# Kernel optimization log

Measured on AMD Instinct MI355X. Metric: run time of the kernel, lower is better.

## Reference

```python
import jax, jax.numpy as jnp
import numpy as np

DIM = 4096
N_EXPERTS = 256
TOPK = 8
N_GROUPS = 8
TOPK_GROUPS = 4
ROUTE_SCALE = 2.5
N_TOKENS = 16384


def setup_inputs() -> dict:
    key = jax.random.key(0)
    k1, k2 = jax.random.split(key)
    x = jax.random.normal(k1, (N_TOKENS, DIM), dtype=jnp.float32)
    weight = jax.random.normal(k2, (N_EXPERTS, DIM), dtype=jnp.float32) * 0.01
    e_score_correction_bias = jnp.zeros((N_EXPERTS,), dtype=jnp.float32)
    return {"x": x, "weight": weight, "e_score_correction_bias": e_score_correction_bias}


def reference(x, weight, e_score_correction_bias):
    n = x.shape[0]
    # [n, E] expert scores
    scores = jax.nn.sigmoid(jnp.dot(x, weight.T))
    original_scores = scores
    scores = scores + e_score_correction_bias
    # group selection: top-2 sum per group -> top-k groups
    scores_g = scores.reshape(n, N_GROUPS, -1)  # [n, G, E/G]
    group_score = jnp.sort(scores_g, axis=-1)[..., -2:].sum(axis=-1)  # [n, G]
    group_idx = jnp.argsort(group_score, axis=-1)[..., -TOPK_GROUPS:]  # [n, kg]
    mask = jnp.ones((n, N_GROUPS), dtype=bool)
    mask = mask.at[jnp.arange(n)[:, None], group_idx].set(False)
    scores_masked = jnp.where(mask[..., None], -jnp.inf, scores_g).reshape(n, -1)
    # final top-k experts
    indices = jnp.argsort(scores_masked, axis=-1)[..., -TOPK:]  # [n, k]
    weights = original_scores[jnp.arange(n)[:, None], indices]  # [n, k]
    weights = weights / (weights.sum(axis=-1, keepdims=True) + 1e-20)
    weights = weights * ROUTE_SCALE
    return (weights, indices)
```

## Files before the change

### kernel.cpp

```cpp
#include <hip/hip_runtime.h>
#include <math.h>

#define DIMK 4096
#define NEXP 256
#define BM   64
#define BK32 32
#define NT   (DIMK / BK32)
#define NGRP 8
#define GSZ  32
#define TOPKG 4
#define TOPKE 8
#define BTILE 49152
#define WS_NEED ((size_t)NT * BTILE)

#define XTILE   12288
#define SMEM_SZ 131584

typedef __bf16 bf16x8 __attribute__((ext_vector_type(8)));
typedef float f32x4 __attribute__((ext_vector_type(4)));

__device__ __forceinline__ void decomp8(const float v[8], uint4& H, uint4& M, uint4& L) {
  union U { __bf16 b[8]; uint4 u; } h, m, l;
#pragma unroll
  for (int i = 0; i < 8; ++i) {
    float xv = v[i];
    __bf16 hb = (__bf16)xv;
    float r1 = xv - (float)hb;
    __bf16 mb = (__bf16)r1;
    float r2 = r1 - (float)mb;
    h.b[i] = hb; m.b[i] = mb; l.b[i] = (__bf16)r2;
  }
  H = h.u; M = m.u; L = l.u;
}

__device__ __forceinline__ void decomp4(float4 v, uint2& H, uint2& M, uint2& L) {
  union U { __bf16 b[4]; uint2 u; } h, m, l;
  float vv[4] = {v.x, v.y, v.z, v.w};
#pragma unroll
  for (int i = 0; i < 4; ++i) {
    float xv = vv[i];
    __bf16 hb = (__bf16)xv;
    float r1 = xv - (float)hb;
    __bf16 mb = (__bf16)r1;
    float r2 = r1 - (float)mb;
    h.b[i] = hb; m.b[i] = mb; l.b[i] = (__bf16)r2;
  }
  H = h.u; M = m.u; L = l.u;
}

__global__ __launch_bounds__(256) void w_split_kernel(const float* __restrict__ wgt,
                                                      unsigned char* __restrict__ ws) {
  const int g = blockIdx.x * 256 + threadIdx.x;
  const int e = g >> 9;
  const int k0 = (g & 511) << 3;
  const int kt = k0 >> 5;
  const int chunk = (k0 & 31) >> 3;
  const int lane = chunk * 16 + (e & 15);
  const int eb = e >> 4;
  float v[8];
  float4 a = *(const float4*)(wgt + (long)e * DIMK + k0);
  float4 b = *(const float4*)(wgt + (long)e * DIMK + k0 + 4);
  v[0]=a.x; v[1]=a.y; v[2]=a.z; v[3]=a.w; v[4]=b.x; v[5]=b.y; v[6]=b.z; v[7]=b.w;
  uint4 H, M, L;
  decomp8(v, H, M, L);
  const long base = ((long)(kt * 3) * 16 + eb) * 1024 + lane * 16;
  *(uint4*)(ws + base)             = H;
  *(uint4*)(ws + base + 16 * 1024) = M;
  *(uint4*)(ws + base + 32 * 1024) = L;
}

__global__ __launch_bounds__(512) void moe_gate_mfma(
    const float* __restrict__ x, const unsigned char* __restrict__ ws,
    const float* __restrict__ bias, float* __restrict__ outw, float* __restrict__ outi) {
  __shared__ __align__(16) unsigned char smem[SMEM_SZ];
  double* sc = (double*)smem;

  const int tid = threadIdx.x;
  const int lane = tid & 63;
  const int l15 = lane & 15;
  const int wid = tid >> 6;
  const int wr = wid >> 2;
  const int wc = wid & 3;
  const long bm0 = (long)blockIdx.x * BM;

  const int xtok = tid >> 3;
  const int xq = tid & 7;
  const float* xptr = x + (bm0 + xtok) * (long)DIMK + xq * 4;
  const int xwoff = (xq >> 1) * 1024 + xtok * 16 + (xq & 1) * 8;

  const unsigned char* wsb = ws + (wc * 4) * 1024 + lane * 16;

  f32x4 D[2][4];
  double acc[2][4][4];
#pragma unroll
  for (int rt = 0; rt < 2; ++rt)
#pragma unroll
    for (int ct = 0; ct < 4; ++ct) {
      D[rt][ct] = (f32x4){0.f, 0.f, 0.f, 0.f};
#pragma unroll
      for (int r = 0; r < 4; ++r) acc[rt][ct][r] = 0.0;
    }

  float4 xv;
  bf16x8 bh0, bh1, bh2, bh3, bm0r, bm1r, bm2r, bm3r, bl0, bl1, bl2, bl3;

  bh0 = *(const bf16x8*)(wsb + 0 * 16384 + 0 * 1024);
  bh1 = *(const bf16x8*)(wsb + 0 * 16384 + 1 * 1024);
  bh2 = *(const bf16x8*)(wsb + 0 * 16384 + 2 * 1024);
  bh3 = *(const bf16x8*)(wsb + 0 * 16384 + 3 * 1024);
  bm0r = *(const bf16x8*)(wsb + 1 * 16384 + 0 * 1024);
  bm1r = *(const bf16x8*)(wsb + 1 * 16384 + 1 * 1024);
  bm2r = *(const bf16x8*)(wsb + 1 * 16384 + 2 * 1024);
  bm3r = *(const bf16x8*)(wsb + 1 * 16384 + 3 * 1024);
  bl0 = *(const bf16x8*)(wsb + 2 * 16384 + 0 * 1024);
  bl1 = *(const bf16x8*)(wsb + 2 * 16384 + 1 * 1024);
  bl2 = *(const bf16x8*)(wsb + 2 * 16384 + 2 * 1024);
  bl3 = *(const bf16x8*)(wsb + 2 * 16384 + 3 * 1024);
  xv = *(const float4*)(xptr);
  {
    uint2 H, M, L;
    decomp4(xv, H, M, L);
    *(uint2*)(smem + xwoff + 0 * 4096) = H;
    *(uint2*)(smem + xwoff + 1 * 4096) = M;
    *(uint2*)(smem + xwoff + 2 * 4096) = L;
  }
  __syncthreads();

#define MM(A, B, RT, CT) \
  D[RT][CT] = __builtin_amdgcn_mfma_f32_16x16x32_bf16(A, B, D[RT][CT], 0, 0, 0)
#define P8(A0, A1, B0, B1, B2, B3) \
  MM(A0, B0, 0, 0); MM(A0, B1, 0, 1); MM(A0, B2, 0, 2); MM(A0, B3, 0, 3); \
  MM(A1, B0, 1, 0); MM(A1, B1, 1, 1); MM(A1, B2, 1, 2); MM(A1, B3, 1, 3)

  long bo_n = BTILE;

#pragma unroll 1
  for (int t = 0; t < NT; ++t) {
    const int buf = t & 1, nbuf = buf ^ 1;
    const bool more = (t + 1 < NT);
    if (more) xv = *(const float4*)(xptr + (t + 1) * BK32);
    const unsigned char* xb = smem + buf * XTILE;
    const int ao0 = (lane >> 4) * 1024 + (wr * 32 + l15) * 16;
    const int ao1 = ao0 + 256;
    bf16x8 ah0 = *(const bf16x8*)(xb + 0 * 4096 + ao0);
    bf16x8 ah1 = *(const bf16x8*)(xb + 0 * 4096 + ao1);
    bf16x8 am0 = *(const bf16x8*)(xb + 1 * 4096 + ao0);
    bf16x8 am1 = *(const bf16x8*)(xb + 1 * 4096 + ao1);
    bf16x8 al0 = *(const bf16x8*)(xb + 2 * 4096 + ao0);
    bf16x8 al1 = *(const bf16x8*)(xb + 2 * 4096 + ao1);
    __builtin_amdgcn_s_setprio(1);
    P8(ah0, ah1, bh0, bh1, bh2, bh3);
    P8(am0, am1, bh0, bh1, bh2, bh3);
    P8(al0, al1, bh0, bh1, bh2, bh3);
    bh0 = *(const bf16x8*)(wsb + bo_n + 0 * 16384 + 0 * 1024);
    bh1 = *(const bf16x8*)(wsb + bo_n + 0 * 16384 + 1 * 1024);
    bh2 = *(const bf16x8*)(wsb + bo_n + 0 * 16384 + 2 * 1024);
    bh3 = *(const bf16x8*)(wsb + bo_n + 0 * 16384 + 3 * 1024);
    P8(ah0, ah1, bm0r, bm1r, bm2r, bm3r);
    P8(am0, am1, bm0r, bm1r, bm2r, bm3r);
    bm0r = *(const bf16x8*)(wsb + bo_n + 1 * 16384 + 0 * 1024);
    bm1r = *(const bf16x8*)(wsb + bo_n + 1 * 16384 + 1 * 1024);
    bm2r = *(const bf16x8*)(wsb + bo_n + 1 * 16384 + 2 * 1024);
    bm3r = *(const bf16x8*)(wsb + bo_n + 1 * 16384 + 3 * 1024);
    P8(ah0, ah1, bl0, bl1, bl2, bl3);
    bl0 = *(const bf16x8*)(wsb + bo_n + 2 * 16384 + 0 * 1024);
    bl1 = *(const bf16x8*)(wsb + bo_n + 2 * 16384 + 1 * 1024);
    bl2 = *(const bf16x8*)(wsb + bo_n + 2 * 16384 + 2 * 1024);
    bl3 = *(const bf16x8*)(wsb + bo_n + 2 * 16384 + 3 * 1024);
    __builtin_amdgcn_s_setprio(0);
    if (more) {
      uint2 H, M, L;
      decomp4(xv, H, M, L);
      unsigned char* xw = smem + nbuf * XTILE + xwoff;
      *(uint2*)(xw + 0 * 4096) = H;
      *(uint2*)(xw + 1 * 4096) = M;
      *(uint2*)(xw + 2 * 4096) = L;
    }
    if (t & 1) {
#pragma unroll
      for (int rt = 0; rt < 2; ++rt)
#pragma unroll
        for (int ct = 0; ct < 4; ++ct) {
#pragma unroll
          for (int r = 0; r < 4; ++r) acc[rt][ct][r] += (double)D[rt][ct][r];
          D[rt][ct] = (f32x4){0.f, 0.f, 0.f, 0.f};
        }
    }
    __syncthreads();
    if (t + 2 < NT) bo_n += BTILE;
  }
#undef P8
#undef MM

#pragma unroll
  for (int rt = 0; rt < 2; ++rt)
#pragma unroll
    for (int ct = 0; ct < 4; ++ct) {
      const int col = wc * 64 + ct * 16 + l15;
      const double bd = (double)bias[col];
#pragma unroll
      for (int r = 0; r < 4; ++r) {
        const int row = wr * 32 + rt * 16 + (lane >> 4) * 4 + r;
        const double s = 1.0 / (1.0 + exp(-acc[rt][ct][r]));
        sc[row * 257 + col] = s + bd;
      }
    }
  __syncthreads();

  if (tid < BM) {
    double* row = sc + tid * 257;
    double gs[NGRP];
#pragma unroll
    for (int g = 0; g < NGRP; ++g) {
      double m1 = -1e300, m2 = -1e300;
      for (int e = 0; e < GSZ; ++e) {
        double v = row[g * GSZ + e];
        if (v > m1) { m2 = m1; m1 = v; }
        else if (v > m2) { m2 = v; }
      }
      gs[g] = m1 + m2;
    }
    unsigned msk = 0;
#pragma unroll
    for (int g = 0; g < NGRP; ++g) {
      int cnt = 0;
#pragma unroll
      for (int h = 0; h < NGRP; ++h)
        cnt += ((gs[h] > gs[g]) || (gs[h] == gs[g] && h > g)) ? 1 : 0;
      if (cnt < TOPKG) msk |= (1u << g);
    }
    int g0 = __ffs(msk) - 1; msk &= msk - 1;
    int g1 = __ffs(msk) - 1; msk &= msk - 1;
    int g2 = __ffs(msk) - 1; msk &= msk - 1;
    int g3 = __ffs(msk) - 1;

    double wv[TOPKE];
    float iv[TOPKE];
#pragma unroll
    for (int r8 = 0; r8 < TOPKE; ++r8) {
      double best = -1e300;
      int bi = 0;
      {
        int gg = g0;
        for (int e = 0; e < GSZ; ++e) { double v = row[gg * GSZ + e]; if (v >= best) { best = v; bi = gg * GSZ + e; } }
        gg = g1;
        for (int e = 0; e < GSZ; ++e) { double v = row[gg * GSZ + e]; if (v >= best) { best = v; bi = gg * GSZ + e; } }
        gg = g2;
        for (int e = 0; e < GSZ; ++e) { double v = row[gg * GSZ + e]; if (v >= best) { best = v; bi = gg * GSZ + e; } }
        gg = g3;
        for (int e = 0; e < GSZ; ++e) { double v = row[gg * GSZ + e]; if (v >= best) { best = v; bi = gg * GSZ + e; } }
      }
      row[bi] = -1e300;
      wv[7 - r8] = best - (double)bias[bi];
      iv[7 - r8] = (float)bi;
    }
    double sum = 0.0;
#pragma unroll
    for (int p = 0; p < TOPKE; ++p) sum += wv[p];
    const double den = sum + 1e-20;
    const long trow = bm0 + tid;
#pragma unroll
    for (int p = 0; p < TOPKE; ++p) {
      outw[trow * 8 + p] = (float)(wv[p] / den * 2.5);
      outi[trow * 8 + p] = iv[p];
    }
  }
}

#define BMF  64
#define BKF 16
#define LXSF 68
__global__ __launch_bounds__(256, 1) void moe_gate_f64(
    const float* __restrict__ x, const float* __restrict__ wgt,
    const float* __restrict__ bias, float* __restrict__ outw,
    float* __restrict__ outi) {
  __shared__ __align__(16) unsigned char smem[64 * 257 * 8];
  float* lw = (float*)smem;
  float* lx = (float*)(smem + 32768);
  double* sc = (double*)smem;
  const int tid = threadIdx.x;
  const long bm0 = (long)blockIdx.x * BMF;
  const int rg = tid >> 5;
  const int cg = tid & 31;
  const int sxr = tid >> 2;
  const int sxj = (tid & 3) << 2;
  const float* xrow = x + (bm0 + sxr) * (long)DIMK + sxj;
  const float* wrow = wgt + (long)tid * DIMK;
  double acc[8][8];
#pragma unroll
  for (int i = 0; i < 8; ++i)
#pragma unroll
    for (int j = 0; j < 8; ++j) acc[i][j] = 0.0;
#define LWF(b, k, e) lw[((b)*BKF + (k)) * NEXP + (e)]
#define LXF(b, k, r) lx[((b)*BKF + (k)) * LXSF + (r)]
  {
    float4 xv = *(const float4*)(xrow);
#pragma unroll
    for (int c = 0; c < 4; ++c) LXF(0, sxj + c, sxr) = ((const float*)&xv)[c];
#pragma unroll
    for (int jj = 0; jj < 4; ++jj) {
      float4 wv = *(const float4*)(wrow + jj * 4);
#pragma unroll
      for (int c = 0; c < 4; ++c) LWF(0, jj * 4 + c, tid) = ((const float*)&wv)[c];
    }
  }
  __syncthreads();
  const int NTF = DIMK / BKF;
  for (int kt = 0; kt < NTF; ++kt) {
    const int b = kt & 1;
    if (kt + 1 < NTF) {
      const int k0 = (kt + 1) * BKF;
      const int nb = b ^ 1;
      float4 xv = *(const float4*)(xrow + k0);
      float4 wv0 = *(const float4*)(wrow + k0);
      float4 wv1 = *(const float4*)(wrow + k0 + 4);
      float4 wv2 = *(const float4*)(wrow + k0 + 8);
      float4 wv3 = *(const float4*)(wrow + k0 + 12);
#pragma unroll
      for (int c = 0; c < 4; ++c) LXF(nb, sxj + c, sxr) = ((const float*)&xv)[c];
#pragma unroll
      for (int c = 0; c < 4; ++c) LWF(nb, 0 + c, tid) = ((const float*)&wv0)[c];
#pragma unroll
      for (int c = 0; c < 4; ++c) LWF(nb, 4 + c, tid) = ((const float*)&wv1)[c];
#pragma unroll
      for (int c = 0; c < 4; ++c) LWF(nb, 8 + c, tid) = ((const float*)&wv2)[c];
#pragma unroll
      for (int c = 0; c < 4; ++c) LWF(nb, 12 + c, tid) = ((const float*)&wv3)[c];
    }
#pragma unroll
    for (int k = 0; k < BKF; ++k) {
      float4 a0 = *(const float4*)(&LXF(b, k, rg * 8));
      float4 a1 = *(const float4*)(&LXF(b, k, rg * 8 + 4));
      double ad[8] = {(double)a0.x, (double)a0.y, (double)a0.z, (double)a0.w,
                      (double)a1.x, (double)a1.y, (double)a1.z, (double)a1.w};
      double bd[8];
#pragma unroll
      for (int j = 0; j < 4; ++j) {
        float2 bb = *(const float2*)(&LWF(b, k, cg * 2 + 64 * j));
        bd[2 * j] = (double)bb.x;
        bd[2 * j + 1] = (double)bb.y;
      }
#pragma unroll
      for (int i = 0; i < 8; ++i)
#pragma unroll
        for (int j = 0; j < 8; ++j) acc[i][j] += ad[i] * bd[j];
    }
    __syncthreads();
  }
  double bc[8];
#pragma unroll
  for (int j = 0; j < 4; ++j) {
    bc[2 * j] = (double)bias[cg * 2 + 64 * j];
    bc[2 * j + 1] = (double)bias[cg * 2 + 64 * j + 1];
  }
#pragma unroll
  for (int i = 0; i < 8; ++i) {
    const int r = rg * 8 + i;
#pragma unroll
    for (int jq = 0; jq < 8; ++jq) {
      const int col = cg * 2 + 64 * (jq >> 1) + (jq & 1);
      double s = 1.0 / (1.0 + exp(-acc[i][jq]));
      sc[r * 257 + col] = s + bc[jq];
    }
  }
  __syncthreads();
  if (tid < BMF) {
    double* row = sc + tid * 257;
    double gs[NGRP];
#pragma unroll
    for (int g = 0; g < NGRP; ++g) {
      double m1 = -1e300, m2 = -1e300;
      for (int e = 0; e < GSZ; ++e) {
        double v = row[g * GSZ + e];
        if (v > m1) { m2 = m1; m1 = v; }
        else if (v > m2) { m2 = v; }
      }
      gs[g] = m1 + m2;
    }
    unsigned msk = 0;
#pragma unroll
    for (int g = 0; g < NGRP; ++g) {
      int cnt = 0;
#pragma unroll
      for (int h = 0; h < NGRP; ++h)
        cnt += ((gs[h] > gs[g]) || (gs[h] == gs[g] && h > g)) ? 1 : 0;
      if (cnt < TOPKG) msk |= (1u << g);
    }
    int g0 = __ffs(msk) - 1; msk &= msk - 1;
    int g1 = __ffs(msk) - 1; msk &= msk - 1;
    int g2 = __ffs(msk) - 1; msk &= msk - 1;
    int g3 = __ffs(msk) - 1;
    double wv[TOPKE];
    float iv[TOPKE];
#pragma unroll
    for (int r8 = 0; r8 < TOPKE; ++r8) {
      double best = -1e300;
      int bi = 0;
      {
        int gg = g0;
        for (int e = 0; e < GSZ; ++e) { double v = row[gg * GSZ + e]; if (v >= best) { best = v; bi = gg * GSZ + e; } }
        gg = g1;
        for (int e = 0; e < GSZ; ++e) { double v = row[gg * GSZ + e]; if (v >= best) { best = v; bi = gg * GSZ + e; } }
        gg = g2;
        for (int e = 0; e < GSZ; ++e) { double v = row[gg * GSZ + e]; if (v >= best) { best = v; bi = gg * GSZ + e; } }
        gg = g3;
        for (int e = 0; e < GSZ; ++e) { double v = row[gg * GSZ + e]; if (v >= best) { best = v; bi = gg * GSZ + e; } }
      }
      row[bi] = -1e300;
      wv[7 - r8] = best - (double)bias[bi];
      iv[7 - r8] = (float)bi;
    }
    double sum = 0.0;
#pragma unroll
    for (int p = 0; p < TOPKE; ++p) sum += wv[p];
    const double den = sum + 1e-20;
    const long trow = bm0 + tid;
#pragma unroll
    for (int p = 0; p < TOPKE; ++p) {
      outw[trow * 8 + p] = (float)(wv[p] / den * 2.5);
      outi[trow * 8 + p] = iv[p];
    }
  }
}

extern "C" void kernel_launch(void* const* d_in, const int* in_sizes, int n_in,
                              void* d_out, int out_size, void* d_ws, size_t ws_size,
                              hipStream_t stream) {
  const float* x = (const float*)d_in[0];
  const float* w = (const float*)d_in[1];
  const float* b = (const float*)d_in[2];
  const int ntok = in_sizes[0] / DIMK;
  float* outw = (float*)d_out;
  float* outi = outw + (size_t)ntok * 8;
  if (ws_size >= WS_NEED) {
    hipLaunchKernelGGL(w_split_kernel, dim3(512), dim3(256), 0, stream,
                       w, (unsigned char*)d_ws);
    hipLaunchKernelGGL(moe_gate_mfma, dim3(ntok / BM), dim3(512), 0, stream,
                       x, (const unsigned char*)d_ws, b, outw, outi);
  } else {
    hipLaunchKernelGGL(moe_gate_f64, dim3(ntok / 64), dim3(256), 0, stream,
                       x, w, b, outw, outi);
  }
}
```

Measured before the change: 228.6 us.

## Double waves per block, one row tile per wave, stream B per tile

Launches 1024 threads per block (16 waves) so each wave computes one 16-row tile across 64 expert columns instead of two row tiles, halving per-wave accumulator registers. The B fragments are no longer prefetched across iterations; each tile's hi/mid/lo planes are loaded in-loop with two register sets. X staging uses 8-float loads by only 256 of the threads. This trades register pressure and per-wave work for more waves, but B traffic per block doubles (each B fragment is fetched by twice as many waves) and load latency is less hidden.

```diff
diff --git a/kernel.cpp b/kernel.cpp
--- a/kernel.cpp
+++ b/kernel.cpp
@@ -13,6 +13,7 @@
 #define BTILE 49152
 #define WS_NEED ((size_t)NT * BTILE)
 
+#define XPLANE  4096
 #define XTILE   12288
 #define SMEM_SZ 131584
 
@@ -24,21 +25,6 @@
 #pragma unroll
   for (int i = 0; i < 8; ++i) {
     float xv = v[i];
-    __bf16 hb = (__bf16)xv;
-    float r1 = xv - (float)hb;
-    __bf16 mb = (__bf16)r1;
-    float r2 = r1 - (float)mb;
-    h.b[i] = hb; m.b[i] = mb; l.b[i] = (__bf16)r2;
-  }
-  H = h.u; M = m.u; L = l.u;
-}
-
-__device__ __forceinline__ void decomp4(float4 v, uint2& H, uint2& M, uint2& L) {
-  union U { __bf16 b[4]; uint2 u; } h, m, l;
-  float vv[4] = {v.x, v.y, v.z, v.w};
-#pragma unroll
-  for (int i = 0; i < 4; ++i) {
-    float xv = vv[i];
     __bf16 hb = (__bf16)xv;
     float r1 = xv - (float)hb;
     __bf16 mb = (__bf16)r1;
@@ -69,7 +55,7 @@
   *(uint4*)(ws + base + 32 * 1024) = L;
 }
 
-__global__ __launch_bounds__(512) void moe_gate_mfma(
+__global__ __launch_bounds__(1024) void moe_gate_mfma(
     const float* __restrict__ x, const unsigned char* __restrict__ ws,
     const float* __restrict__ bias, float* __restrict__ outw, float* __restrict__ outi) {
   __shared__ __align__(16) unsigned char smem[SMEM_SZ];
@@ -83,128 +69,110 @@
   const int wc = wid & 3;
   const long bm0 = (long)blockIdx.x * BM;
 
-  const int xtok = tid >> 3;
-  const int xq = tid & 7;
-  const float* xptr = x + (bm0 + xtok) * (long)DIMK + xq * 4;
-  const int xwoff = (xq >> 1) * 1024 + xtok * 16 + (xq & 1) * 8;
+  const int xtok = tid >> 2;
+  const int xch = tid & 3;
+  const bool stager = (tid < 256);
+  const float* xptr = x + (bm0 + xtok) * (long)DIMK + xch * 8;
+  const int xwoff = xch * 1024 + xtok * 16;
 
   const unsigned char* wsb = ws + (wc * 4) * 1024 + lane * 16;
 
-  f32x4 D[2][4];
-  double acc[2][4][4];
-#pragma unroll
-  for (int rt = 0; rt < 2; ++rt)
-#pragma unroll
-    for (int ct = 0; ct < 4; ++ct) {
-      D[rt][ct] = (f32x4){0.f, 0.f, 0.f, 0.f};
-#pragma unroll
-      for (int r = 0; r < 4; ++r) acc[rt][ct][r] = 0.0;
-    }
-
-  float4 xv;
-  bf16x8 bh0, bh1, bh2, bh3, bm0r, bm1r, bm2r, bm3r, bl0, bl1, bl2, bl3;
-
-  bh0 = *(const bf16x8*)(wsb + 0 * 16384 + 0 * 1024);
-  bh1 = *(const bf16x8*)(wsb + 0 * 16384 + 1 * 1024);
-  bh2 = *(const bf16x8*)(wsb + 0 * 16384 + 2 * 1024);
-  bh3 = *(const bf16x8*)(wsb + 0 * 16384 + 3 * 1024);
-  bm0r = *(const bf16x8*)(wsb + 1 * 16384 + 0 * 1024);
-  bm1r = *(const bf16x8*)(wsb + 1 * 16384 + 1 * 1024);
-  bm2r = *(const bf16x8*)(wsb + 1 * 16384 + 2 * 1024);
-  bm3r = *(const bf16x8*)(wsb + 1 * 16384 + 3 * 1024);
-  bl0 = *(const bf16x8*)(wsb + 2 * 16384 + 0 * 1024);
-  bl1 = *(const bf16x8*)(wsb + 2 * 16384 + 1 * 1024);
-  bl2 = *(const bf16x8*)(wsb + 2 * 16384 + 2 * 1024);
-  bl3 = *(const bf16x8*)(wsb + 2 * 16384 + 3 * 1024);
-  xv = *(const float4*)(xptr);
-  {
-    uint2 H, M, L;
-    decomp4(xv, H, M, L);
-    *(uint2*)(smem + xwoff + 0 * 4096) = H;
-    *(uint2*)(smem + xwoff + 1 * 4096) = M;
-    *(uint2*)(smem + xwoff + 2 * 4096) = L;
+  f32x4 D[4];
+  double acc[4][4];
+#pragma unroll
+  for (int ct = 0; ct < 4; ++ct) {
+    D[ct] = (f32x4){0.f, 0.f, 0.f, 0.f};
+#pragma unroll
+    for (int r = 0; r < 4; ++r) acc[ct][r] = 0.0;
+  }
+
+  float4 xa, xb4;
+
+  if (stager) {
+    xa = *(const float4*)(xptr);
+    xb4 = *(const float4*)(xptr + 4);
+    float v[8] = {xa.x, xa.y, xa.z, xa.w, xb4.x, xb4.y, xb4.z, xb4.w};
+    uint4 H, M, L;
+    decomp8(v, H, M, L);
+    *(uint4*)(smem + 0 * XPLANE + xwoff) = H;
+    *(uint4*)(smem + 1 * XPLANE + xwoff) = M;
+    *(uint4*)(smem + 2 * XPLANE + xwoff) = L;
   }
   __syncthreads();
 
-#define MM(A, B, RT, CT) \
-  D[RT][CT] = __builtin_amdgcn_mfma_f32_16x16x32_bf16(A, B, D[RT][CT], 0, 0, 0)
-#define P8(A0, A1, B0, B1, B2, B3) \
-  MM(A0, B0, 0, 0); MM(A0, B1, 0, 1); MM(A0, B2, 0, 2); MM(A0, B3, 0, 3); \
-  MM(A1, B0, 1, 0); MM(A1, B1, 1, 1); MM(A1, B2, 1, 2); MM(A1, B3, 1, 3)
-
-  long bo_n = BTILE;
+#define MM(A, B, CT) \
+  D[CT] = __builtin_amdgcn_mfma_f32_16x16x32_bf16(A, B, D[CT], 0, 0, 0)
+#define P4(A, B0, B1, B2, B3) \
+  MM(A, B0, 0); MM(A, B1, 1); MM(A, B2, 2); MM(A, B3, 3)
 
 #pragma unroll 1
   for (int t = 0; t < NT; ++t) {
     const int buf = t & 1, nbuf = buf ^ 1;
     const bool more = (t + 1 < NT);
-    if (more) xv = *(const float4*)(xptr + (t + 1) * BK32);
-    const unsigned char* xb = smem + buf * XTILE;
-    const int ao0 = (lane >> 4) * 1024 + (wr * 32 + l15) * 16;
-    const int ao1 = ao0 + 256;
-    bf16x8 ah0 = *(const bf16x8*)(xb + 0 * 4096 + ao0);
-    bf16x8 ah1 = *(const bf16x8*)(xb + 0 * 4096 + ao1);
-    bf16x8 am0 = *(const bf16x8*)(xb + 1 * 4096 + ao0);
-    bf16x8 am1 = *(const bf16x8*)(xb + 1 * 4096 + ao1);
-    bf16x8 al0 = *(const bf16x8*)(xb + 2 * 4096 + ao0);
-    bf16x8 al1 = *(const bf16x8*)(xb + 2 * 4096 + ao1);
+    if (more && stager) {
+      xa = *(const float4*)(xptr + (t + 1) * BK32);
+      xb4 = *(const float4*)(xptr + (t + 1) * BK32 + 4);
+    }
+    const unsigned char* xbuf = smem + buf * XTILE;
+    const int ao = (lane >> 4) * 1024 + (wr * 16 + l15) * 16;
+    bf16x8 ah = *(const bf16x8*)(xbuf + 0 * XPLANE + ao);
+    bf16x8 am = *(const bf16x8*)(xbuf + 1 * XPLANE + ao);
+    bf16x8 al = *(const bf16x8*)(xbuf + 2 * XPLANE + ao);
+    const unsigned char* bt = wsb + (long)t * BTILE;
+    bf16x8 pA0, pA1, pA2, pA3, pB0, pB1, pB2, pB3;
     __builtin_amdgcn_s_setprio(1);
-    P8(ah0, ah1, bh0, bh1, bh2, bh3);
-    P8(am0, am1, bh0, bh1, bh2, bh3);
-    P8(al0, al1, bh0, bh1, bh2, bh3);
-    bh0 = *(const bf16x8*)(wsb + bo_n + 0 * 16384 + 0 * 1024);
-    bh1 = *(const bf16x8*)(wsb + bo_n + 0 * 16384 + 1 * 1024);
-    bh2 = *(const bf16x8*)(wsb + bo_n + 0 * 16384 + 2 * 1024);
-    bh3 = *(const bf16x8*)(wsb + bo_n + 0 * 16384 + 3 * 1024);
-    P8(ah0, ah1, bm0r, bm1r, bm2r, bm3r);
-    P8(am0, am1, bm0r, bm1r, bm2r, bm3r);
-    bm0r = *(const bf16x8*)(wsb + bo_n + 1 * 16384 + 0 * 1024);
-    bm1r = *(const bf16x8*)(wsb + bo_n + 1 * 16384 + 1 * 1024);
-    bm2r = *(const bf16x8*)(wsb + bo_n + 1 * 16384 + 2 * 1024);
-    bm3r = *(const bf16x8*)(wsb + bo_n + 1 * 16384 + 3 * 1024);
-    P8(ah0, ah1, bl0, bl1, bl2, bl3);
-    bl0 = *(const bf16x8*)(wsb + bo_n + 2 * 16384 + 0 * 1024);
-    bl1 = *(const bf16x8*)(wsb + bo_n + 2 * 16384 + 1 * 1024);
-    bl2 = *(const bf16x8*)(wsb + bo_n + 2 * 16384 + 2 * 1024);
-    bl3 = *(const bf16x8*)(wsb + bo_n + 2 * 16384 + 3 * 1024);
+    pA0 = *(const bf16x8*)(bt + 0 * 16384 + 0 * 1024);
+    pA1 = *(const bf16x8*)(bt + 0 * 16384 + 1 * 1024);
+    pA2 = *(const bf16x8*)(bt + 0 * 16384 + 2 * 1024);
+    pA3 = *(const bf16x8*)(bt + 0 * 16384 + 3 * 1024);
+    P4(ah, pA0, pA1, pA2, pA3);
+    P4(am, pA0, pA1, pA2, pA3);
+    pB0 = *(const bf16x8*)(bt + 1 * 16384 + 0 * 1024);
+    pB1 = *(const bf16x8*)(bt + 1 * 16384 + 1 * 1024);
+    pB2 = *(const bf16x8*)(bt + 1 * 16384 + 2 * 1024);
+    pB3 = *(const bf16x8*)(bt + 1 * 16384 + 3 * 1024);
+    P4(al, pA0, pA1, pA2, pA3);
+    pA0 = *(const bf16x8*)(bt + 2 * 16384 + 0 * 1024);
+    pA1 = *(const bf16x8*)(bt + 2 * 16384 + 1 * 1024);
+    pA2 = *(const bf16x8*)(bt + 2 * 16384 + 2 * 1024);
+    pA3 = *(const bf16x8*)(bt + 2 * 16384 + 3 * 1024);
+    P4(ah, pB0, pB1, pB2, pB3);
+    P4(am, pB0, pB1, pB2, pB3);
+    P4(ah, pA0, pA1, pA2, pA3);
     __builtin_amdgcn_s_setprio(0);
-    if (more) {
-      uint2 H, M, L;
-      decomp4(xv, H, M, L);
+    if (more && stager) {
+      float v[8] = {xa.x, xa.y, xa.z, xa.w, xb4.x, xb4.y, xb4.z, xb4.w};
+      uint4 H, M, L;
+      decomp8(v, H, M, L);
       unsigned char* xw = smem + nbuf * XTILE + xwoff;
-      *(uint2*)(xw + 0 * 4096) = H;
-      *(uint2*)(xw + 1 * 4096) = M;
-      *(uint2*)(xw + 2 * 4096) = L;
+      *(uint4*)(xw + 0 * XPLANE) = H;
+      *(uint4*)(xw + 1 * XPLANE) = M;
+      *(uint4*)(xw + 2 * XPLANE) = L;
     }
     if (t & 1) {
 #pragma unroll
-      for (int rt = 0; rt < 2; ++rt)
-#pragma unroll
-        for (int ct = 0; ct < 4; ++ct) {
-#pragma unroll
-          for (int r = 0; r < 4; ++r) acc[rt][ct][r] += (double)D[rt][ct][r];
-          D[rt][ct] = (f32x4){0.f, 0.f, 0.f, 0.f};
-        }
+      for (int ct = 0; ct < 4; ++ct) {
+#pragma unroll
+        for (int r = 0; r < 4; ++r) acc[ct][r] += (double)D[ct][r];
+        D[ct] = (f32x4){0.f, 0.f, 0.f, 0.f};
+      }
     }
     __syncthreads();
-    if (t + 2 < NT) bo_n += BTILE;
-  }
-#undef P8
+  }
+#undef P4
 #undef MM
 
 #pragma unroll
-  for (int rt = 0; rt < 2; ++rt)
-#pragma unroll
-    for (int ct = 0; ct < 4; ++ct) {
-      const int col = wc * 64 + ct * 16 + l15;
-      const double bd = (double)bias[col];
-#pragma unroll
-      for (int r = 0; r < 4; ++r) {
-        const int row = wr * 32 + rt * 16 + (lane >> 4) * 4 + r;
-        const double s = 1.0 / (1.0 + exp(-acc[rt][ct][r]));
-        sc[row * 257 + col] = s + bd;
-      }
-    }
+  for (int ct = 0; ct < 4; ++ct) {
+    const int col = wc * 64 + ct * 16 + l15;
+    const double bd = (double)bias[col];
+#pragma unroll
+    for (int r = 0; r < 4; ++r) {
+      const int row = wr * 16 + (lane >> 4) * 4 + r;
+      const double s = 1.0 / (1.0 + exp(-acc[ct][r]));
+      sc[row * 257 + col] = s + bd;
+    }
+  }
   __syncthreads();
 
   if (tid < BM) {
@@ -435,7 +403,7 @@
   if (ws_size >= WS_NEED) {
     hipLaunchKernelGGL(w_split_kernel, dim3(512), dim3(256), 0, stream,
                        w, (unsigned char*)d_ws);
-    hipLaunchKernelGGL(moe_gate_mfma, dim3(ntok / BM), dim3(512), 0, stream,
+    hipLaunchKernelGGL(moe_gate_mfma, dim3(ntok / BM), dim3(1024), 0, stream,
                        x, (const unsigned char*)d_ws, b, outw, outi);
   } else {
     hipLaunchKernelGGL(moe_gate_f64, dim3(ntok / 64), dim3(256), 0, stream,
```

After: 326.9 us. 1.43x slower.
